# Performance work log

Measured on AMD Instinct MI355X. Metric: run time of the kernel, lower is better.

Reference implementation:

```python
import jax, jax.numpy as jnp
import numpy as np

NEG_SLOPE = 0.2  # PyG GATv2Conv default negative_slope
NUM_GRAPHS = 512


def _gatv2_layer(x, Wl, Wr, att, bias, src, dst, n):
    # GATv2: e_ij = att . LeakyReLU(Wl x_j + Wr x_i); softmax over incoming edges of i
    xl = x @ Wl                      # [N, H] source transform
    xr = x @ Wr                      # [N, H] target transform
    e = jax.nn.leaky_relu(xl[src] + xr[dst], NEG_SLOPE)  # [E, H]
    logits = e @ att                 # [E]
    m = jax.ops.segment_max(logits, dst, num_segments=n)
    a = jnp.exp(logits - m[dst])
    denom = jax.ops.segment_sum(a, dst, num_segments=n)
    a = a / denom[dst]               # segment softmax (every node has a self loop)
    out = jax.ops.segment_sum(a[:, None] * xl[src], dst, num_segments=n)
    return out + bias


def setup_inputs() -> dict:
    key = jax.random.key(0)
    ks = jax.random.split(key, 12)
    N, E, Cin, H, Cout = 100000, 3200000, 19, 32, 4
    x = jax.random.normal(ks[0], (N, Cin), dtype=jnp.float32)
    edge_index = jax.random.randint(ks[1], (2, E), 0, N, dtype=jnp.int64)
    batch = jnp.sort(jax.random.randint(ks[2], (N,), 0, NUM_GRAPHS, dtype=jnp.int64))
    s = 0.1
    return {
        "x": x,
        "edge_index": edge_index,
        "batch": batch,
        "Wl1": jax.random.normal(ks[3], (Cin, H), dtype=jnp.float32) * s,
        "Wr1": jax.random.normal(ks[4], (Cin, H), dtype=jnp.float32) * s,
        "att1": jax.random.normal(ks[5], (H,), dtype=jnp.float32) * s,
        "b1": jnp.zeros((H,), dtype=jnp.float32),
        "Wl2": jax.random.normal(ks[6], (H, H), dtype=jnp.float32) * s,
        "Wr2": jax.random.normal(ks[7], (H, H), dtype=jnp.float32) * s,
        "att2": jax.random.normal(ks[8], (H,), dtype=jnp.float32) * s,
        "b2": jnp.zeros((H,), dtype=jnp.float32),
        "Wlin": jax.random.normal(ks[9], (H, Cout), dtype=jnp.float32) * s,
        "blin": jnp.zeros((Cout,), dtype=jnp.float32),
    }


def reference(x, edge_index, batch, Wl1, Wr1, att1, b1, Wl2, Wr2, att2, b2, Wlin, blin):
    n = x.shape[0]
    loops = jnp.arange(n, dtype=edge_index.dtype)  # add_self_loops=True (PyG default)
    src = jnp.concatenate([edge_index[0], loops])
    dst = jnp.concatenate([edge_index[1], loops])
    h = jax.nn.relu(_gatv2_layer(x, Wl1, Wr1, att1, b1, src, dst, n))
    h = jax.nn.relu(_gatv2_layer(h, Wl2, Wr2, att2, b2, src, dst, n))
    # global_mean_pool over graph ids
    sums = jax.ops.segment_sum(h, batch, num_segments=NUM_GRAPHS)
    cnt = jax.ops.segment_sum(jnp.ones((n,), h.dtype), batch, num_segments=NUM_GRAPHS)
    features = sums / jnp.maximum(cnt, 1.0)[:, None]
    logits = features @ Wlin + blin
    return logits, features
```

## Files before the change

kernel.cpp:

```cpp
#include <hip/hip_runtime.h>
#include <cstdint>
#include <cstddef>

#define WG 256
#define NPB 256
#define NPB_SHIFT 8
#define CAP 9216
#define BIN_CHUNK 4096

typedef _Float16 half4 __attribute__((ext_vector_type(4)));


__global__ __launch_bounds__(512) void k_front(
        const int* __restrict__ esrc, const int* __restrict__ edst,
        int* __restrict__ gcnt, unsigned* __restrict__ staging,
        int E, int NB, int binBlocks,
        const float* __restrict__ x, const float* __restrict__ Wl,
        const float* __restrict__ Wr, _Float16* __restrict__ xl,
        _Float16* __restrict__ xr, int N, int Cin, int linBlocks,
        const int* __restrict__ batch, int* __restrict__ gstart, int G) {
    __shared__ unsigned sval[BIN_CHUNK];
    __shared__ unsigned short sbkt[BIN_CHUNK];
    __shared__ int hist[512];
    __shared__ int cursor[512];
    __shared__ int gbase[512];
    __shared__ int wtot[8];
    __shared__ int stotal;

    int t = threadIdx.x;

    if (blockIdx.x < (unsigned)binBlocks) {
        hist[t] = 0;
        __syncthreads();
        long base = (long)blockIdx.x * BIN_CHUNK;
        int vb[BIN_CHUNK / 512];
        unsigned vv[BIN_CHUNK / 512];
#pragma unroll
        for (int k = 0; k < BIN_CHUNK / 512; k++) {
            long e = base + k * 512 + t;
            int b = -1; unsigned v = 0;
            if (e < E) {
                int d = edst[e];
                b = d >> NPB_SHIFT;
                v = ((unsigned)esrc[e] << NPB_SHIFT) | (unsigned)(d & (NPB - 1));
                atomicAdd(&hist[b], 1);
            }
            vb[k] = b; vv[k] = v;
        }
        __syncthreads();
        int lane = t & 63, wvq = t >> 6;
        int c = hist[t];
        int v = c;
#pragma unroll
        for (int off = 1; off < 64; off <<= 1) {
            int u = __shfl_up(v, off);
            if (lane >= off) v += u;
        }
        if (lane == 63) wtot[wvq] = v;
        __syncthreads();
        int add = 0;
#pragma unroll
        for (int wq = 0; wq < 8; wq++) add += (wq < wvq) ? wtot[wq] : 0;
        int incl = v + add;
        int st = incl - c;
        cursor[t] = st;
        if (t == 511) stotal = incl;
        int wb = 0;
        if (t < NB && c > 0) wb = atomicAdd(&gcnt[t], c);
        gbase[t] = wb + t * CAP - st;
        __syncthreads();
#pragma unroll
        for (int k = 0; k < BIN_CHUNK / 512; k++) {
            int b = vb[k];
            if (b >= 0) {
                int r = atomicAdd(&cursor[b], 1);
                sval[r] = vv[k];
                sbkt[r] = (unsigned short)b;
            }
        }
        __syncthreads();
        int total = stotal;
        for (int j = t; j < total; j += 512) {
            int b = sbkt[j];
            int addr = gbase[b] + j;
            if (addr < (b + 1) * CAP)
                staging[addr] = sval[j];
        }
    } else if (blockIdx.x < (unsigned)(binBlocks + linBlocks)) {
        float* sl = (float*)sval;
        float* sr = (float*)sval + 1024;
        float* sx = (float*)sval + 2048;
        int bb = blockIdx.x - binBlocks;
        for (int i = t; i < Cin * 32; i += 512) { sl[i] = Wl[i]; sr[i] = Wr[i]; }
        int n0 = bb * 16;
        int cnt = min(16, N - n0);
        for (int i = t; i < cnt * Cin; i += 512) sx[i] = x[(long)n0 * Cin + i];
        __syncthreads();
        int n = t >> 5, h = t & 31;
        if (n < cnt) {
            float al = 0.f, ar = 0.f;
            for (int k = 0; k < Cin; k++) {
                float xv = sx[n * Cin + k];
                al = fmaf(xv, sl[k * 32 + h], al);
                ar = fmaf(xv, sr[k * 32 + h], ar);
            }
            xl[(long)(n0 + n) * 32 + h] = (_Float16)al;
            xr[(long)(n0 + n) * 32 + h] = (_Float16)ar;
        }
    } else {
        int g = (blockIdx.x - binBlocks - linBlocks) * 512 + t;
        if (g <= G) {
            int lo = 0, hi = N;
            while (lo < hi) {
                int mid = (lo + hi) >> 1;
                if (batch[mid] < g) lo = mid + 1; else hi = mid;
            }
            gstart[g] = lo;
        }
    }
}

__global__ __launch_bounds__(512) void k_bucket(const unsigned* __restrict__ staging,
                                                const int* __restrict__ gcnt,
                                                int* __restrict__ offsets,
                                                int* __restrict__ csr_src,
                                                int N, int NB) {
    __shared__ unsigned sslab[CAP];
    __shared__ int hist[NPB];
    __shared__ int cur[NPB];
    __shared__ int wtot[8];
    int b = blockIdx.x;
    int t = threadIdx.x;
    int lane = t & 63, wv = t >> 6;

    int a = 0;
    for (int j = t; j < b; j += 512)
        a += min(gcnt[j], CAP) + min(NPB, N - j * NPB);
#pragma unroll
    for (int off = 1; off < 64; off <<= 1) a += __shfl_xor(a, off);
    if (lane == 0) wtot[wv] = a;
    if (t < NPB) hist[t] = 0;
    __syncthreads();
    int bbase = wtot[0] + wtot[1] + wtot[2] + wtot[3]
              + wtot[4] + wtot[5] + wtot[6] + wtot[7];

    int cnt = min(gcnt[b], CAP);
    const unsigned* slab = staging + (long)b * CAP;
    for (int j = t; j < cnt; j += 512) {
        unsigned e = slab[j];
        sslab[j] = e;
        atomicAdd(&hist[e & (NPB - 1)], 1);
    }
    if (b == NB - 1 && t == 0)
        offsets[N] = bbase + cnt + min(NPB, N - b * NPB);
    __syncthreads();

    int node = b * NPB + t;
    int c = 0, v = 0;
    if (t < NPB) {
        c = (node < N) ? hist[t] + 1 : 0;
        v = c;
#pragma unroll
        for (int off = 1; off < 64; off <<= 1) {
            int u = __shfl_up(v, off);
            if (lane >= off) v += u;
        }
        if (lane == 63) wtot[wv] = v;
    }
    __syncthreads();
    if (t < NPB) {
        int add = (wv >= 1 ? wtot[0] : 0) + (wv >= 2 ? wtot[1] : 0)
                + (wv >= 3 ? wtot[2] : 0);
        int o = bbase + (v + add) - c;
        if (node < N) {
            offsets[node] = o;
            csr_src[o] = node;
            cur[t] = o + 1;
        }
    }
    __syncthreads();
    for (int j = t; j < cnt; j += 512) {
        unsigned e = sslab[j];
        int p = atomicAdd(&cur[e & (NPB - 1)], 1);
        csr_src[p] = (int)(e >> NPB_SHIFT);
    }
}

__global__ __launch_bounds__(512) void k_lin(const float* __restrict__ x,
                                             const float* __restrict__ Wl,
                                             const float* __restrict__ Wr,
                                             _Float16* __restrict__ xl,
                                             _Float16* __restrict__ xr,
                                             int N, int Cin) {
    __shared__ float sl[1024];
    __shared__ float sr[1024];
    __shared__ float sx[512];
    int t = threadIdx.x;
    for (int i = t; i < Cin * 32; i += 512) { sl[i] = Wl[i]; sr[i] = Wr[i]; }
    int n0 = blockIdx.x * 16;
    int cnt = min(16, N - n0);
    for (int i = t; i < cnt * Cin; i += 512) sx[i] = x[(long)n0 * Cin + i];
    __syncthreads();
    int n = t >> 5, h = t & 31;
    if (n >= cnt) return;
    float al = 0.f, ar = 0.f;
    for (int k = 0; k < Cin; k++) {
        float xv = sx[n * Cin + k];
        al = fmaf(xv, sl[k * 32 + h], al);
        ar = fmaf(xv, sr[k * 32 + h], ar);
    }
    xl[(long)(n0 + n) * 32 + h] = (_Float16)al;
    xr[(long)(n0 + n) * 32 + h] = (_Float16)ar;
}

__global__ __launch_bounds__(WG) void k_gat(
        const _Float16* __restrict__ xl, const _Float16* __restrict__ xr,
        const int* __restrict__ offsets, const int* __restrict__ csr,
        const float* __restrict__ att, const float* __restrict__ bias,
        float* __restrict__ out, int N) {
    int lane = threadIdx.x & 63;
    int wid = blockIdx.x * (WG / 64) + (threadIdx.x >> 6);
    int iA = wid * 2;
    if (iA >= N) return;
    int iB = iA + 1;
    int e8 = lane >> 3;
    int hq = lane & 7;
    unsigned hq8 = (unsigned)hq << 3;

    const char* xlb = (const char*)xl;
    const char* csrb = (const char*)csr;

    int startA = offsets[iA], endA = offsets[iA + 1];
    int startB = 0, endB = 0;
    if (iB < N) { startB = endA; endB = offsets[iB + 1]; }

    float4 att4 = *(const float4*)(att + hq * 4);
    const float L2E = 1.4426950408889634f;
    att4.x *= L2E; att4.y *= L2E; att4.z *= L2E; att4.w *= L2E;

    const _Float16 ns = (_Float16)0.2f;
    half4 hzero = {(_Float16)0.f, (_Float16)0.f, (_Float16)0.f, (_Float16)0.f};

    half4 xrA = *(const half4*)(xr + (long)iA * 32 + hq * 4);
    half4 xrB = hzero;
    if (iB < N) xrB = *(const half4*)(xr + (long)iB * 32 + hq * 4);

    float denomA = 0.f, denomB = 0.f;
    float4 accA = {0.f, 0.f, 0.f, 0.f};
    float4 accB = {0.f, 0.f, 0.f, 0.f};

    int itA = (endA - startA + 7) >> 3;
    int itB = (endB - startB + 7) >> 3;
    int iters = max(itA, itB);

    int pA = startA + e8, pB = startB + e8;
    int sA = -1, sB = -1;
    if (pA < endA) sA = *(const int*)(csrb + ((unsigned)pA << 2));
    if (pB < endB) sB = *(const int*)(csrb + ((unsigned)pB << 2));

    for (int it = 0; it < iters; ++it) {
        half4 xa = hzero;
        half4 xb = hzero;
        if (sA >= 0) xa = *(const half4*)(xlb + (((unsigned)sA << 6) | hq8));
        if (sB >= 0) xb = *(const half4*)(xlb + (((unsigned)sB << 6) | hq8));
        pA += 8; pB += 8;
        int sA2 = -1, sB2 = -1;
        if (pA < endA) sA2 = *(const int*)(csrb + ((unsigned)pA << 2));
        if (pB < endB) sB2 = *(const int*)(csrb + ((unsigned)pB << 2));

        {
            half4 s = xa + xrA;
            half4 m = s * ns;
            half4 tt = __builtin_elementwise_max(s, m);
            float l = fmaf((float)tt[0], att4.x,
                      fmaf((float)tt[1], att4.y,
                      fmaf((float)tt[2], att4.z,
                           (float)tt[3] * att4.w)));
            l += __shfl_xor(l, 1);
            l += __shfl_xor(l, 2);
            l += __shfl_xor(l, 4);
            float wA = __builtin_amdgcn_exp2f(l);
            wA = (sA >= 0) ? wA : 0.f;
            denomA += wA;
            accA.x = fmaf(wA, (float)xa[0], accA.x);
            accA.y = fmaf(wA, (float)xa[1], accA.y);
            accA.z = fmaf(wA, (float)xa[2], accA.z);
            accA.w = fmaf(wA, (float)xa[3], accA.w);
        }
        {
            half4 s = xb + xrB;
            half4 m = s * ns;
            half4 tt = __builtin_elementwise_max(s, m);
            float l = fmaf((float)tt[0], att4.x,
                      fmaf((float)tt[1], att4.y,
                      fmaf((float)tt[2], att4.z,
                           (float)tt[3] * att4.w)));
            l += __shfl_xor(l, 1);
            l += __shfl_xor(l, 2);
            l += __shfl_xor(l, 4);
            float wB = __builtin_amdgcn_exp2f(l);
            wB = (sB >= 0) ? wB : 0.f;
            denomB += wB;
            accB.x = fmaf(wB, (float)xb[0], accB.x);
            accB.y = fmaf(wB, (float)xb[1], accB.y);
            accB.z = fmaf(wB, (float)xb[2], accB.z);
            accB.w = fmaf(wB, (float)xb[3], accB.w);
        }
        sA = sA2; sB = sB2;
    }

    denomA += __shfl_xor(denomA, 8); denomA += __shfl_xor(denomA, 16); denomA += __shfl_xor(denomA, 32);
    denomB += __shfl_xor(denomB, 8); denomB += __shfl_xor(denomB, 16); denomB += __shfl_xor(denomB, 32);
    accA.x += __shfl_xor(accA.x, 8); accA.x += __shfl_xor(accA.x, 16); accA.x += __shfl_xor(accA.x, 32);
    accA.y += __shfl_xor(accA.y, 8); accA.y += __shfl_xor(accA.y, 16); accA.y += __shfl_xor(accA.y, 32);
    accA.z += __shfl_xor(accA.z, 8); accA.z += __shfl_xor(accA.z, 16); accA.z += __shfl_xor(accA.z, 32);
    accA.w += __shfl_xor(accA.w, 8); accA.w += __shfl_xor(accA.w, 16); accA.w += __shfl_xor(accA.w, 32);
    accB.x += __shfl_xor(accB.x, 8); accB.x += __shfl_xor(accB.x, 16); accB.x += __shfl_xor(accB.x, 32);
    accB.y += __shfl_xor(accB.y, 8); accB.y += __shfl_xor(accB.y, 16); accB.y += __shfl_xor(accB.y, 32);
    accB.z += __shfl_xor(accB.z, 8); accB.z += __shfl_xor(accB.z, 16); accB.z += __shfl_xor(accB.z, 32);
    accB.w += __shfl_xor(accB.w, 8); accB.w += __shfl_xor(accB.w, 16); accB.w += __shfl_xor(accB.w, 32);

    const float4 b4 = *(const float4*)(bias + hq * 4);
    if (lane < 8) {
        float inv = 1.0f / denomA;
        float4 o;
        o.x = fmaxf(fmaf(accA.x, inv, b4.x), 0.f);
        o.y = fmaxf(fmaf(accA.y, inv, b4.y), 0.f);
        o.z = fmaxf(fmaf(accA.z, inv, b4.z), 0.f);
        o.w = fmaxf(fmaf(accA.w, inv, b4.w), 0.f);
        *(float4*)(out + (long)iA * 32 + hq * 4) = o;
    } else if (lane < 16 && iB < N) {
        float inv = 1.0f / denomB;
        float4 o;
        o.x = fmaxf(fmaf(accB.x, inv, b4.x), 0.f);
        o.y = fmaxf(fmaf(accB.y, inv, b4.y), 0.f);
        o.z = fmaxf(fmaf(accB.z, inv, b4.z), 0.f);
        o.w = fmaxf(fmaf(accB.w, inv, b4.w), 0.f);
        *(float4*)(out + (long)iB * 32 + hq * 4) = o;
    }
}

__global__ __launch_bounds__(WG) void k_pool(const float* __restrict__ h2v,
                                             const int* __restrict__ gstart,
                                             const float* __restrict__ Wlin,
                                             const float* __restrict__ blin,
                                             float* __restrict__ out, int G) {
    __shared__ float red[WG];
    int g = blockIdx.x;
    int t = threadIdx.x;
    int h = t & 31;
    int grp = t >> 5;
    int s = gstart[g], e = gstart[g + 1];
    float acc = 0.f;
    for (int n = s + grp; n < e; n += 8)
        acc += h2v[(long)n * 32 + h];
    red[t] = acc;
    __syncthreads();
    if (grp == 0) {
        float a = red[h] + red[h + 32] + red[h + 64] + red[h + 96]
                + red[h + 128] + red[h + 160] + red[h + 192] + red[h + 224];
        int cnt = e - s;
        float c = (float)(cnt > 1 ? cnt : 1);
        float f = a / c;
        out[G * 4 + g * 32 + h] = f;
        float p0 = f * Wlin[h * 4 + 0];
        float p1 = f * Wlin[h * 4 + 1];
        float p2 = f * Wlin[h * 4 + 2];
        float p3 = f * Wlin[h * 4 + 3];
        for (int off = 1; off < 32; off <<= 1) {
            p0 += __shfl_xor(p0, off);
            p1 += __shfl_xor(p1, off);
            p2 += __shfl_xor(p2, off);
            p3 += __shfl_xor(p3, off);
        }
        if (h == 0) {
            out[g * 4 + 0] = p0 + blin[0];
            out[g * 4 + 1] = p1 + blin[1];
            out[g * 4 + 2] = p2 + blin[2];
            out[g * 4 + 3] = p3 + blin[3];
        }
    }
}

extern "C" void kernel_launch(void* const* d_in, const int* in_sizes, int n_in,
                              void* d_out, int out_size, void* d_ws, size_t ws_size,
                              hipStream_t stream) {
    const float* x    = (const float*)d_in[0];
    const int*   ei   = (const int*)d_in[1];
    const int*   batch= (const int*)d_in[2];
    const float* Wl1  = (const float*)d_in[3];
    const float* Wr1  = (const float*)d_in[4];
    const float* att1 = (const float*)d_in[5];
    const float* b1   = (const float*)d_in[6];
    const float* Wl2  = (const float*)d_in[7];
    const float* Wr2  = (const float*)d_in[8];
    const float* att2 = (const float*)d_in[9];
    const float* b2   = (const float*)d_in[10];
    const float* Wlin = (const float*)d_in[11];
    const float* blin = (const float*)d_in[12];
    float* out = (float*)d_out;

    const int N   = in_sizes[2];
    const int Cin = in_sizes[0] / N;
    const int E   = in_sizes[1] / 2;
    const int G   = out_size / 36;
    const int* src = ei;
    const int* dst = ei + E;
    const int NB  = (N + NPB - 1) >> NPB_SHIFT;

    char* w = (char*)d_ws;
    auto alloc = [&](size_t bytes) {
        char* p = w;
        w += (bytes + 255) & ~(size_t)255;
        return p;
    };
    int* offsets = (int*)alloc((size_t)(N + 1) * 4);
    int* gstart  = (int*)alloc((size_t)(G + 1) * 4);
    int* gcnt    = (int*)alloc((size_t)NB * 4);
    int* csr_src = (int*)alloc((size_t)(E + N) * 4);
    unsigned* staging = (unsigned*)alloc((size_t)NB * CAP * 4);
    _Float16* xl = (_Float16*)alloc((size_t)N * 32 * 2);
    _Float16* xr = (_Float16*)alloc((size_t)N * 32 * 2);
    float* h1    = (float*)alloc((size_t)N * 32 * 4);
    float* h2v   = h1;

    hipMemsetAsync(gcnt, 0, (size_t)NB * 4, stream);

    int binBlocks = (E + BIN_CHUNK - 1) / BIN_CHUNK;
    int linBlocks = ((long)N * 32 + 511) / 512;
    int stBlocks  = (G + 1 + 511) / 512;

    k_front<<<binBlocks + linBlocks + stBlocks, 512, 0, stream>>>(
        src, dst, gcnt, staging, E, NB, binBlocks,
        x, Wl1, Wr1, xl, xr, N, Cin, linBlocks,
        batch, gstart, G);

    k_bucket<<<NB, 512, 0, stream>>>(staging, gcnt, offsets, csr_src, N, NB);

    int waves = (N + 1) / 2;
    int gat_grid = (waves + 3) / 4;

    k_gat<<<gat_grid, WG, 0, stream>>>(xl, xr, offsets, csr_src, att1, b1, h1, N);

    k_lin<<<linBlocks, 512, 0, stream>>>(h1, Wl2, Wr2, xl, xr, N, 32);
    k_gat<<<gat_grid, WG, 0, stream>>>(xl, xr, offsets, csr_src, att2, b2, h2v, N);

    k_pool<<<G, WG, 0, stream>>>(h2v, gstart, Wlin, blin, out, G);
}
```

Before: 283.3 us.

## Software-pipeline gathered features in GAT loop and drop LDS staging in linear transform

Result: slower. 305.5 us (+7.8%).

```diff
diff --git a/kernel.cpp b/kernel.cpp
--- a/kernel.cpp
+++ b/kernel.cpp
@@ -10,6 +10,46 @@
 
 typedef _Float16 half4 __attribute__((ext_vector_type(4)));
 
+
+template <int CIN>
+__device__ __forceinline__ void lin_node(const float* __restrict__ x,
+                                         const float* __restrict__ Wl,
+                                         const float* __restrict__ Wr,
+                                         _Float16* __restrict__ xl,
+                                         _Float16* __restrict__ xr,
+                                         long n, int h) {
+    const float* xp = x + n * CIN;
+    float al = 0.f, ar = 0.f;
+#pragma unroll
+    for (int k = 0; k < CIN; k++) {
+        float xv = xp[k];
+        al = fmaf(xv, Wl[k * 32 + h], al);
+        ar = fmaf(xv, Wr[k * 32 + h], ar);
+    }
+    xl[n * 32 + h] = (_Float16)al;
+    xr[n * 32 + h] = (_Float16)ar;
+}
+
+__device__ __forceinline__ void lin_dispatch(const float* __restrict__ x,
+                                             const float* __restrict__ Wl,
+                                             const float* __restrict__ Wr,
+                                             _Float16* __restrict__ xl,
+                                             _Float16* __restrict__ xr,
+                                             long n, int h, int Cin) {
+    if (Cin == 19)      lin_node<19>(x, Wl, Wr, xl, xr, n, h);
+    else if (Cin == 32) lin_node<32>(x, Wl, Wr, xl, xr, n, h);
+    else {
+        const float* xp = x + (long)n * Cin;
+        float al = 0.f, ar = 0.f;
+        for (int k = 0; k < Cin; k++) {
+            float xv = xp[k];
+            al = fmaf(xv, Wl[k * 32 + h], al);
+            ar = fmaf(xv, Wr[k * 32 + h], ar);
+        }
+        xl[n * 32 + h] = (_Float16)al;
+        xr[n * 32 + h] = (_Float16)ar;
+    }
+}
 
 __global__ __launch_bounds__(512) void k_front(
         const int* __restrict__ esrc, const int* __restrict__ edst,
@@ -87,26 +127,10 @@
                 staging[addr] = sval[j];
         }
     } else if (blockIdx.x < (unsigned)(binBlocks + linBlocks)) {
-        float* sl = (float*)sval;
-        float* sr = (float*)sval + 1024;
-        float* sx = (float*)sval + 2048;
-        int bb = blockIdx.x - binBlocks;
-        for (int i = t; i < Cin * 32; i += 512) { sl[i] = Wl[i]; sr[i] = Wr[i]; }
-        int n0 = bb * 16;
-        int cnt = min(16, N - n0);
-        for (int i = t; i < cnt * Cin; i += 512) sx[i] = x[(long)n0 * Cin + i];
-        __syncthreads();
-        int n = t >> 5, h = t & 31;
-        if (n < cnt) {
-            float al = 0.f, ar = 0.f;
-            for (int k = 0; k < Cin; k++) {
-                float xv = sx[n * Cin + k];
-                al = fmaf(xv, sl[k * 32 + h], al);
-                ar = fmaf(xv, sr[k * 32 + h], ar);
-            }
-            xl[(long)(n0 + n) * 32 + h] = (_Float16)al;
-            xr[(long)(n0 + n) * 32 + h] = (_Float16)ar;
-        }
+        long idx = (long)(blockIdx.x - binBlocks) * 512 + t;
+        long n = idx >> 5;
+        int h = (int)(idx & 31);
+        if (n < N) lin_dispatch(x, Wl, Wr, xl, xr, n, h, Cin);
     } else {
         int g = (blockIdx.x - binBlocks - linBlocks) * 512 + t;
         if (g <= G) {
@@ -192,25 +216,11 @@
                                              _Float16* __restrict__ xl,
                                              _Float16* __restrict__ xr,
                                              int N, int Cin) {
-    __shared__ float sl[1024];
-    __shared__ float sr[1024];
-    __shared__ float sx[512];
-    int t = threadIdx.x;
-    for (int i = t; i < Cin * 32; i += 512) { sl[i] = Wl[i]; sr[i] = Wr[i]; }
-    int n0 = blockIdx.x * 16;
-    int cnt = min(16, N - n0);
-    for (int i = t; i < cnt * Cin; i += 512) sx[i] = x[(long)n0 * Cin + i];
-    __syncthreads();
-    int n = t >> 5, h = t & 31;
-    if (n >= cnt) return;
-    float al = 0.f, ar = 0.f;
-    for (int k = 0; k < Cin; k++) {
-        float xv = sx[n * Cin + k];
-        al = fmaf(xv, sl[k * 32 + h], al);
-        ar = fmaf(xv, sr[k * 32 + h], ar);
-    }
-    xl[(long)(n0 + n) * 32 + h] = (_Float16)al;
-    xr[(long)(n0 + n) * 32 + h] = (_Float16)ar;
+    long idx = (long)blockIdx.x * 512 + threadIdx.x;
+    long n = idx >> 5;
+    int h = (int)(idx & 31);
+    if (n >= N) return;
+    lin_dispatch(x, Wl, Wr, xl, xr, n, h, Cin);
 }
 
 __global__ __launch_bounds__(WG) void k_gat(
@@ -254,22 +264,28 @@
     int iters = max(itA, itB);
 
     int pA = startA + e8, pB = startB + e8;
-    int sA = -1, sB = -1;
-    if (pA < endA) sA = *(const int*)(csrb + ((unsigned)pA << 2));
-    if (pB < endB) sB = *(const int*)(csrb + ((unsigned)pB << 2));
+    int sA0 = -1, sB0 = -1;
+    if (pA < endA) sA0 = *(const int*)(csrb + ((unsigned)pA << 2));
+    if (pB < endB) sB0 = *(const int*)(csrb + ((unsigned)pB << 2));
+    pA += 8; pB += 8;
+    int sA1 = -1, sB1 = -1;
+    if (pA < endA) sA1 = *(const int*)(csrb + ((unsigned)pA << 2));
+    if (pB < endB) sB1 = *(const int*)(csrb + ((unsigned)pB << 2));
+    half4 xa0 = hzero, xb0 = hzero;
+    if (sA0 >= 0) xa0 = *(const half4*)(xlb + (((unsigned)sA0 << 6) | hq8));
+    if (sB0 >= 0) xb0 = *(const half4*)(xlb + (((unsigned)sB0 << 6) | hq8));
 
     for (int it = 0; it < iters; ++it) {
-        half4 xa = hzero;
-        half4 xb = hzero;
-        if (sA >= 0) xa = *(const half4*)(xlb + (((unsigned)sA << 6) | hq8));
-        if (sB >= 0) xb = *(const half4*)(xlb + (((unsigned)sB << 6) | hq8));
+        half4 xa1 = hzero, xb1 = hzero;
+        if (sA1 >= 0) xa1 = *(const half4*)(xlb + (((unsigned)sA1 << 6) | hq8));
+        if (sB1 >= 0) xb1 = *(const half4*)(xlb + (((unsigned)sB1 << 6) | hq8));
         pA += 8; pB += 8;
         int sA2 = -1, sB2 = -1;
         if (pA < endA) sA2 = *(const int*)(csrb + ((unsigned)pA << 2));
         if (pB < endB) sB2 = *(const int*)(csrb + ((unsigned)pB << 2));
 
         {
-            half4 s = xa + xrA;
+            half4 s = xa0 + xrA;
             half4 m = s * ns;
             half4 tt = __builtin_elementwise_max(s, m);
             float l = fmaf((float)tt[0], att4.x,
@@ -280,15 +296,15 @@
             l += __shfl_xor(l, 2);
             l += __shfl_xor(l, 4);
             float wA = __builtin_amdgcn_exp2f(l);
-            wA = (sA >= 0) ? wA : 0.f;
+            wA = (sA0 >= 0) ? wA : 0.f;
             denomA += wA;
-            accA.x = fmaf(wA, (float)xa[0], accA.x);
-            accA.y = fmaf(wA, (float)xa[1], accA.y);
-            accA.z = fmaf(wA, (float)xa[2], accA.z);
-            accA.w = fmaf(wA, (float)xa[3], accA.w);
+            accA.x = fmaf(wA, (float)xa0[0], accA.x);
+            accA.y = fmaf(wA, (float)xa0[1], accA.y);
+            accA.z = fmaf(wA, (float)xa0[2], accA.z);
+            accA.w = fmaf(wA, (float)xa0[3], accA.w);
         }
         {
-            half4 s = xb + xrB;
+            half4 s = xb0 + xrB;
             half4 m = s * ns;
             half4 tt = __builtin_elementwise_max(s, m);
             float l = fmaf((float)tt[0], att4.x,
@@ -299,14 +315,15 @@
             l += __shfl_xor(l, 2);
             l += __shfl_xor(l, 4);
             float wB = __builtin_amdgcn_exp2f(l);
-            wB = (sB >= 0) ? wB : 0.f;
+            wB = (sB0 >= 0) ? wB : 0.f;
             denomB += wB;
-            accB.x = fmaf(wB, (float)xb[0], accB.x);
-            accB.y = fmaf(wB, (float)xb[1], accB.y);
-            accB.z = fmaf(wB, (float)xb[2], accB.z);
-            accB.w = fmaf(wB, (float)xb[3], accB.w);
-        }
-        sA = sA2; sB = sB2;
+            accB.x = fmaf(wB, (float)xb0[0], accB.x);
+            accB.y = fmaf(wB, (float)xb0[1], accB.y);
+            accB.z = fmaf(wB, (float)xb0[2], accB.z);
+            accB.w = fmaf(wB, (float)xb0[3], accB.w);
+        }
+        sA0 = sA1; sB0 = sB1; sA1 = sA2; sB1 = sB2;
+        xa0 = xa1; xb0 = xb1;
     }
 
     denomA += __shfl_xor(denomA, 8); denomA += __shfl_xor(denomA, 16); denomA += __shfl_xor(denomA, 32);
```
